# Performance work log

Measured on AMD Instinct MI355X. Metric: run time of the kernel, lower is better.

## Reference

```python
import jax, jax.numpy as jnp
import numpy as np

B, S, IN, H = 16, 512, 512, 256
TAU_TRACE = 20.0
TAU_MEM = 20.0
DECAY_TRACE = float(np.exp(-1.0 / TAU_TRACE))  # exp_convolve decay
DECAY_MEM = float(np.exp(-1.0 / TAU_MEM))      # leaky-integrator dynamics decay
LR = 0.01                                       # plasticity learning rate
W_MAX = 1.0                                     # soft upper bound on fast weights


def setup_inputs() -> dict:
    key = jax.random.key(0)
    k1, k2 = jax.random.split(key)
    x = jax.random.normal(k1, (B, S, IN), dtype=jnp.float32)
    # xavier_uniform with gain=sqrt(2) on W of shape [2H, IN]
    lim = float(np.sqrt(2.0) * np.sqrt(6.0 / (2 * H + IN)))
    W = jax.random.uniform(k2, (2 * H, IN), dtype=jnp.float32, minval=-lim, maxval=lim)
    return {"x": x, "W": W}


def reference(x, W):
    # i = x @ W^T : [B, S, 2H], then split into key/value input currents
    i = jnp.einsum('bsi,hi->bsh', x, W)
    ik, iv = jnp.split(i, 2, axis=2)  # each [B, S, H]
    bsz = x.shape[0]
    h = W.shape[0] // 2

    def step(carry, inp):
        kv, vv, kt, vt, mem = carry
        ik_t, iv_t = inp  # [B, H] each
        # key dynamics (leaky integrator + tanh)
        kv = DECAY_MEM * kv + ik_t
        key = jnp.tanh(kv)
        # memory readout: 0.2 * (key.unsqueeze(1) * mem).sum(2) == 0.2 * mem @ key
        ikv = 0.2 * jnp.einsum('bij,bj->bi', mem, key)
        # value dynamics
        vv = DECAY_MEM * vv + iv_t + ikv
        val = jnp.tanh(vv)
        # exponential traces
        kt = DECAY_TRACE * kt + (1.0 - DECAY_TRACE) * key
        vt = DECAY_TRACE * vt + (1.0 - DECAY_TRACE) * val
        # soft-bounded Hebbian outer-product fast-weight update
        mem = mem + LR * (vt[:, :, None] * kt[:, None, :]) * (W_MAX - mem)
        return (kv, vv, kt, vt, mem), (key, val)

    z = jnp.zeros((bsz, h), x.dtype)
    mem0 = jnp.zeros((bsz, h, h), x.dtype)
    (_, _, _, _, mem), (keys, vals) = jax.lax.scan(
        step, (z, z, z, z, mem0),
        (jnp.swapaxes(ik, 0, 1), jnp.swapaxes(iv, 0, 1)))  # scan over time
    return mem, jnp.swapaxes(keys, 0, 1), jnp.swapaxes(vals, 0, 1)
```

## Files before the change

### kernel.cpp

```cpp
#include <hip/hip_runtime.h>

#define BB 16
#define SS 512
#define KIN 512
#define H 256

typedef float v2f __attribute__((ext_vector_type(2)));

constexpr float DECAY = 0.951229424500714f;
constexpr float OMD   = 0.048770575499286f;
constexpr float LR    = 0.01f;

__device__ __forceinline__ float fast_tanh(float x) {
    float e = __expf(2.f * x);
    return 1.f - __fdividef(2.f, e + 1.f);
}

__device__ __forceinline__ v2f pk_mul(v2f a, v2f b) {
    v2f d; asm("v_pk_mul_f32 %0, %1, %2" : "=v"(d) : "v"(a), "v"(b)); return d;
}
__device__ __forceinline__ v2f pk_fma(v2f a, v2f b, v2f c) {
    v2f d; asm("v_pk_fma_f32 %0, %1, %2, %3" : "=v"(d) : "v"(a), "v"(b), "v"(c)); return d;
}

__device__ __forceinline__ void half_sum32(float x, float& s_lo, float& s_hi) {
    int t;
    t = __builtin_amdgcn_update_dpp(0, __float_as_int(x), 0x111, 0xf, 0xf, false);
    x += __int_as_float(t);
    t = __builtin_amdgcn_update_dpp(0, __float_as_int(x), 0x112, 0xf, 0xf, false);
    x += __int_as_float(t);
    t = __builtin_amdgcn_update_dpp(0, __float_as_int(x), 0x114, 0xf, 0xf, false);
    x += __int_as_float(t);
    t = __builtin_amdgcn_update_dpp(0, __float_as_int(x), 0x118, 0xf, 0xf, false);
    x += __int_as_float(t);
    t = __builtin_amdgcn_update_dpp(0, __float_as_int(x), 0x142, 0xa, 0xf, false);
    x += __int_as_float(t);
    s_lo = __int_as_float(__builtin_amdgcn_readlane(__float_as_int(x), 31));
    s_hi = __int_as_float(__builtin_amdgcn_readlane(__float_as_int(x), 63));
}

__global__ __launch_bounds__(256) void gemm_xwT(const float* __restrict__ X,
                                                const float* __restrict__ W,
                                                float* __restrict__ ik_out,
                                                float* __restrict__ iv_t) {
    __shared__ float As[16][68];
    __shared__ float Bs[16][68];
    const int m0 = blockIdx.y * 64;
    const int n0 = blockIdx.x * 64;
    const int tid = threadIdx.x;
    const int r  = tid >> 2;
    const int cg = tid & 3;
    const int tx = tid & 15;
    const int ty = tid >> 4;
    float acc[4][4] = {};
    for (int k0 = 0; k0 < KIN; k0 += 16) {
        float4 av = *(const float4*)&X[(size_t)(m0 + r) * KIN + k0 + cg * 4];
        float4 bv = *(const float4*)&W[(size_t)(n0 + r) * KIN + k0 + cg * 4];
        __syncthreads();
        As[cg*4+0][r] = av.x; As[cg*4+1][r] = av.y; As[cg*4+2][r] = av.z; As[cg*4+3][r] = av.w;
        Bs[cg*4+0][r] = bv.x; Bs[cg*4+1][r] = bv.y; Bs[cg*4+2][r] = bv.z; Bs[cg*4+3][r] = bv.w;
        __syncthreads();
#pragma unroll
        for (int kk = 0; kk < 16; ++kk) {
            float4 a = *(const float4*)&As[kk][ty * 4];
            float4 b = *(const float4*)&Bs[kk][tx * 4];
            float ar[4] = {a.x, a.y, a.z, a.w};
            float br[4] = {b.x, b.y, b.z, b.w};
#pragma unroll
            for (int i = 0; i < 4; ++i)
#pragma unroll
                for (int j = 0; j < 4; ++j) acc[i][j] += ar[i] * br[j];
        }
    }
    if (n0 < 256) {
#pragma unroll
        for (int i = 0; i < 4; ++i) {
            float4 o = make_float4(acc[i][0], acc[i][1], acc[i][2], acc[i][3]);
            *(float4*)&ik_out[(size_t)(m0 + ty * 4 + i) * 256 + n0 + tx * 4] = o;
        }
    } else {
        const int b  = m0 >> 9;
        const int s0 = (m0 & 511) + ty * 4;
#pragma unroll
        for (int j = 0; j < 4; ++j) {
            float4 o = make_float4(acc[0][j], acc[1][j], acc[2][j], acc[3][j]);
            *(float4*)&iv_t[((size_t)b * H + (n0 - 256 + tx * 4 + j)) * SS + s0] = o;
        }
    }
}

__global__ __launch_bounds__(64) void key_scan(const float* __restrict__ ik,
                                               float* __restrict__ keys) {
    const int idx = blockIdx.x * 64 + threadIdx.x;
    const int b   = idx >> 8;
    const int col = idx & 255;
    const float* c  = ik + (size_t)b * SS * 256 + col;
    float* ko = keys + (size_t)b * SS * H + col;
    float kv = 0.f;
    constexpr int D = 32;
    float ib[D];
#pragma unroll
    for (int j = 0; j < D; ++j) ib[j] = c[(size_t)j * 256];
    for (int t = 0; t < SS; t += D) {
#pragma unroll
        for (int j = 0; j < D; ++j) {
            float v = ib[j];
            int tn = t + D + j; if (tn > SS - 1) tn = SS - 1;
            ib[j] = c[(size_t)tn * 256];
            kv = DECAY * kv + v;
            ko[(size_t)(t + j) * H] = fast_tanh(kv);
        }
    }
}

__global__ __launch_bounds__(256) void value_scan(const float* __restrict__ keys,
                                                  const float* __restrict__ iv_t,
                                                  float* __restrict__ mem_out,
                                                  float* __restrict__ vals) {
    const int tid  = threadIdx.x;
    const int wave = tid >> 6;
    const int lane = tid & 63;
    const int half = lane >> 5;
    const int sub  = lane & 31;
    const int b    = blockIdx.x & 15;
    const int rg   = blockIdx.x >> 4;
    const int row  = rg * 8 + wave * 2 + half;
    const int so   = sub * 8;

    const float* kp  = keys + (size_t)b * SS * H + so;
    const float* ivp = iv_t + ((size_t)b * H + row) * SS;
    float* vrow = vals + (size_t)b * SS * H + row;

    const v2f DEC2 = {DECAY, DECAY};
    const v2f OMD2 = {OMD, OMD};
    const v2f ONE2 = {1.f, 1.f};
    const v2f NM12 = {-1.f, -1.f};

    v2f mem2[4] = {{0.f,0.f},{0.f,0.f},{0.f,0.f},{0.f,0.f}};
    v2f ktr[4]  = {{0.f,0.f},{0.f,0.f},{0.f,0.f},{0.f,0.f}};
    float vv = 0.f, vt = 0.f, stash = 0.f;

    v2f kR[8][4];
#pragma unroll
    for (int j = 0; j < 8; ++j)
#pragma unroll
        for (int q = 0; q < 4; ++q)
            kR[j][q] = *(const v2f*)(kp + (size_t)j * H + q * 2);
    kp += 8 * H;

    float4 ivA0 = *(const float4*)(ivp);
    float4 ivA1 = *(const float4*)(ivp + 4);
    float4 ivB0 = *(const float4*)(ivp + 8);
    float4 ivB1 = *(const float4*)(ivp + 12);
    ivp += 16;

#define VS_STEP(J, RELOAD, KOFF)                                               \
    {                                                                          \
        const int SL = (J) & 7;                                                \
        v2f kc0 = kR[SL][0], kc1 = kR[SL][1], kc2 = kR[SL][2], kc3 = kR[SL][3];\
        if (RELOAD) {                                                          \
            kR[SL][0] = *(const v2f*)(kp + (KOFF) * H + 0);                    \
            kR[SL][1] = *(const v2f*)(kp + (KOFF) * H + 2);                    \
            kR[SL][2] = *(const v2f*)(kp + (KOFF) * H + 4);                    \
            kR[SL][3] = *(const v2f*)(kp + (KOFF) * H + 6);                    \
        }                                                                      \
        v2f p2 = pk_mul(mem2[0], kc0);                                         \
        p2 = pk_fma(mem2[1], kc1, p2);                                         \
        p2 = pk_fma(mem2[2], kc2, p2);                                         \
        p2 = pk_fma(mem2[3], kc3, p2);                                         \
        float slo, shi;                                                        \
        half_sum32(p2.x + p2.y, slo, shi);                                     \
        float ps = half ? shi : slo;                                           \
        float civ = ivs[J];                                                    \
        vv = __builtin_fmaf(DECAY, vv, civ);                                   \
        vv = __builtin_fmaf(0.2f, ps, vv);                                     \
        float valv = fast_tanh(vv);                                            \
        vt = __builtin_fmaf(DECAY, vt, OMD * valv);                            \
        if (sub == (J)) stash = valv;                                          \
        float c = LR * vt;                                                     \
        v2f c2 = {c, c};                                                       \
        ktr[0] = pk_fma(DEC2, ktr[0], pk_mul(OMD2, kc0));                      \
        ktr[1] = pk_fma(DEC2, ktr[1], pk_mul(OMD2, kc1));                      \
        ktr[2] = pk_fma(DEC2, ktr[2], pk_mul(OMD2, kc2));                      \
        ktr[3] = pk_fma(DEC2, ktr[3], pk_mul(OMD2, kc3));                      \
        v2f d0 = pk_fma(mem2[0], NM12, ONE2);                                  \
        v2f d1 = pk_fma(mem2[1], NM12, ONE2);                                  \
        v2f d2 = pk_fma(mem2[2], NM12, ONE2);                                  \
        v2f d3 = pk_fma(mem2[3], NM12, ONE2);                                  \
        mem2[0] = pk_fma(pk_mul(c2, ktr[0]), d0, mem2[0]);                     \
        mem2[1] = pk_fma(pk_mul(c2, ktr[1]), d1, mem2[1]);                     \
        mem2[2] = pk_fma(pk_mul(c2, ktr[2]), d2, mem2[2]);                     \
        mem2[3] = pk_fma(pk_mul(c2, ktr[3]), d3, mem2[3]);                     \
    }

#define VS_TILE16(RELOAD_A, RELOAD_B)                                          \
    {                                                                          \
        float ivs[16] = {ivA0.x, ivA0.y, ivA0.z, ivA0.w,                       \
                         ivA1.x, ivA1.y, ivA1.z, ivA1.w,                       \
                         ivB0.x, ivB0.y, ivB0.z, ivB0.w,                       \
                         ivB1.x, ivB1.y, ivB1.z, ivB1.w};                      \
        VS_STEP(0, RELOAD_A, 0) VS_STEP(1, RELOAD_A, 1)                        \
        VS_STEP(2, RELOAD_A, 2) VS_STEP(3, RELOAD_A, 3)                        \
        if (RELOAD_A) kp += 4 * H;                                             \
        VS_STEP(4, RELOAD_A, 0) VS_STEP(5, RELOAD_A, 1)                        \
        VS_STEP(6, RELOAD_A, 2) VS_STEP(7, RELOAD_A, 3)                        \
        if (RELOAD_A) kp += 4 * H;                                             \
        VS_STEP(8, RELOAD_B, 0) VS_STEP(9, RELOAD_B, 1)                        \
        VS_STEP(10, RELOAD_B, 2) VS_STEP(11, RELOAD_B, 3)                      \
        if (RELOAD_B) kp += 4 * H;                                             \
        VS_STEP(12, RELOAD_B, 0) VS_STEP(13, RELOAD_B, 1)                      \
        VS_STEP(14, RELOAD_B, 2) VS_STEP(15, RELOAD_B, 3)                      \
        if (RELOAD_B) kp += 4 * H;                                             \
        if (sub < 16) vrow[(size_t)sub * H] = stash;                           \
        vrow += 16 * H;                                                        \
    }

    for (int t0 = 0; t0 < SS - 16; t0 += 16) {
        float4 nA0 = *(const float4*)(ivp);
        float4 nA1 = *(const float4*)(ivp + 4);
        float4 nB0 = *(const float4*)(ivp + 8);
        float4 nB1 = *(const float4*)(ivp + 12);
        ivp += 16;
        VS_TILE16(true, true)
        ivA0 = nA0; ivA1 = nA1; ivB0 = nB0; ivB1 = nB1;
    }
    VS_TILE16(true, false)
#undef VS_TILE16
#undef VS_STEP

    float* mo = &mem_out[((size_t)b * H + row) * H + so];
    *(float4*)&mo[0] = make_float4(mem2[0].x, mem2[0].y, mem2[1].x, mem2[1].y);
    *(float4*)&mo[4] = make_float4(mem2[2].x, mem2[2].y, mem2[3].x, mem2[3].y);
}

extern "C" void kernel_launch(void* const* d_in, const int* in_sizes, int n_in,
                              void* d_out, int out_size, void* d_ws, size_t ws_size,
                              hipStream_t stream) {
    const float* x = (const float*)d_in[0];
    const float* W = (const float*)d_in[1];
    float* out = (float*)d_out;
    float* mem_out = out;
    float* keys = out + (size_t)BB * H * H;
    float* vals = keys + (size_t)BB * SS * H;
    float* ik   = (float*)d_ws;
    float* iv_t = ik + (size_t)BB * SS * 256;

    dim3 gb(8, 128);
    gemm_xwT<<<gb, 256, 0, stream>>>(x, W, ik, iv_t);
    key_scan<<<64, 64, 0, stream>>>(ik, keys);
    value_scan<<<512, 256, 0, stream>>>(keys, iv_t, mem_out, vals);
}
```

Before: 255.1 us.

## Stage key tiles through double-buffered LDS in value_scan instead of per-lane global reloads

The value scan now loads each 16-step tile of keys once per block with coalesced float4 global loads. It writes the tile into a double-buffered shared-memory array in a permuted layout, and each lane reads its 8-element key slice from LDS through a two-slot register ring. Before, every lane kept an 8-step register window and reloaded its slice from global memory, so the 8 rows of a block fetched the same keys redundantly. The change also adds a __syncthreads per tile and a minimum-occupancy hint of 2 blocks per SM. These cost barrier stalls and LDS latency on the serial recurrence, and may constrain register allocation.

```diff
diff --git a/kernel.cpp b/kernel.cpp
--- a/kernel.cpp
+++ b/kernel.cpp
@@ -113,10 +113,11 @@
     }
 }
 
-__global__ __launch_bounds__(256) void value_scan(const float* __restrict__ keys,
-                                                  const float* __restrict__ iv_t,
-                                                  float* __restrict__ mem_out,
-                                                  float* __restrict__ vals) {
+__global__ __launch_bounds__(256, 2) void value_scan(const float* __restrict__ keys,
+                                                     const float* __restrict__ iv_t,
+                                                     float* __restrict__ mem_out,
+                                                     float* __restrict__ vals) {
+    __shared__ float klds[2][16][256];
     const int tid  = threadIdx.x;
     const int wave = tid >> 6;
     const int lane = tid & 63;
@@ -125,9 +126,13 @@
     const int b    = blockIdx.x & 15;
     const int rg   = blockIdx.x >> 4;
     const int row  = rg * 8 + wave * 2 + half;
-    const int so   = sub * 8;
-
-    const float* kp  = keys + (size_t)b * SS * H + so;
+    const int sub2 = sub * 2;
+    const int lane4 = lane * 4;
+    const int s2   = (lane >> 1) * 2;
+    const int q2a  = (lane * 2) & 3;
+    const int q2b  = (lane * 2 + 1) & 3;
+
+    const float* kb  = keys + (size_t)b * SS * H;
     const float* ivp = iv_t + ((size_t)b * H + row) * SS;
     float* vrow = vals + (size_t)b * SS * H + row;
 
@@ -139,31 +144,42 @@
     v2f mem2[4] = {{0.f,0.f},{0.f,0.f},{0.f,0.f},{0.f,0.f}};
     v2f ktr[4]  = {{0.f,0.f},{0.f,0.f},{0.f,0.f},{0.f,0.f}};
     float vv = 0.f, vt = 0.f, stash = 0.f;
-
-    v2f kR[8][4];
-#pragma unroll
-    for (int j = 0; j < 8; ++j)
-#pragma unroll
-        for (int q = 0; q < 4; ++q)
-            kR[j][q] = *(const v2f*)(kp + (size_t)j * H + q * 2);
-    kp += 8 * H;
-
-    float4 ivA0 = *(const float4*)(ivp);
-    float4 ivA1 = *(const float4*)(ivp + 4);
-    float4 ivB0 = *(const float4*)(ivp + 8);
-    float4 ivB1 = *(const float4*)(ivp + 12);
-    ivp += 16;
-
-#define VS_STEP(J, RELOAD, KOFF)                                               \
+    v2f ring[2][4];
+    float4 g0, g1, g2, g3;
+
+#define LOADG(TI) {                                                            \
+        const float* gp_ = kb + (size_t)((TI) * 16 + wave * 4) * H + lane4;    \
+        g0 = *(const float4*)(gp_);                                            \
+        g1 = *(const float4*)(gp_ + H);                                        \
+        g2 = *(const float4*)(gp_ + 2 * H);                                    \
+        g3 = *(const float4*)(gp_ + 3 * H);                                    \
+    }
+
+#define STAGE(BUF) {                                                           \
+        float* rb_ = &klds[BUF][wave * 4][0];                                  \
+        *(v2f*)(rb_ + q2a * 64 + s2)       = v2f{g0.x, g0.y};                  \
+        *(v2f*)(rb_ + q2b * 64 + s2)       = v2f{g0.z, g0.w};                  \
+        *(v2f*)(rb_ + 256 + q2a * 64 + s2) = v2f{g1.x, g1.y};                  \
+        *(v2f*)(rb_ + 256 + q2b * 64 + s2) = v2f{g1.z, g1.w};                  \
+        *(v2f*)(rb_ + 512 + q2a * 64 + s2) = v2f{g2.x, g2.y};                  \
+        *(v2f*)(rb_ + 512 + q2b * 64 + s2) = v2f{g2.z, g2.w};                  \
+        *(v2f*)(rb_ + 768 + q2a * 64 + s2) = v2f{g3.x, g3.y};                  \
+        *(v2f*)(rb_ + 768 + q2b * 64 + s2) = v2f{g3.z, g3.w};                  \
+    }
+
+#define RD(J, SLOT) {                                                          \
+        const float* r_ = &klds[cur][J][sub2];                                 \
+        ring[SLOT][0] = *(const v2f*)(r_);                                     \
+        ring[SLOT][1] = *(const v2f*)(r_ + 64);                                \
+        ring[SLOT][2] = *(const v2f*)(r_ + 128);                               \
+        ring[SLOT][3] = *(const v2f*)(r_ + 192);                               \
+    }
+
+#define VS_STEP(J)                                                             \
     {                                                                          \
-        const int SL = (J) & 7;                                                \
-        v2f kc0 = kR[SL][0], kc1 = kR[SL][1], kc2 = kR[SL][2], kc3 = kR[SL][3];\
-        if (RELOAD) {                                                          \
-            kR[SL][0] = *(const v2f*)(kp + (KOFF) * H + 0);                    \
-            kR[SL][1] = *(const v2f*)(kp + (KOFF) * H + 2);                    \
-            kR[SL][2] = *(const v2f*)(kp + (KOFF) * H + 4);                    \
-            kR[SL][3] = *(const v2f*)(kp + (KOFF) * H + 6);                    \
-        }                                                                      \
+        v2f kc0 = ring[(J)&1][0], kc1 = ring[(J)&1][1],                        \
+            kc2 = ring[(J)&1][2], kc3 = ring[(J)&1][3];                        \
+        if ((J) < 14) RD((J) + 2, (J)&1);                                      \
         v2f p2 = pk_mul(mem2[0], kc0);                                         \
         p2 = pk_fma(mem2[1], kc1, p2);                                         \
         p2 = pk_fma(mem2[2], kc2, p2);                                         \
@@ -171,8 +187,7 @@
         float slo, shi;                                                        \
         half_sum32(p2.x + p2.y, slo, shi);                                     \
         float ps = half ? shi : slo;                                           \
-        float civ = ivs[J];                                                    \
-        vv = __builtin_fmaf(DECAY, vv, civ);                                   \
+        vv = __builtin_fmaf(DECAY, vv, ivs[J]);                                \
         vv = __builtin_fmaf(0.2f, ps, vv);                                     \
         float valv = fast_tanh(vv);                                            \
         vt = __builtin_fmaf(DECAY, vt, OMD * valv);                            \
@@ -193,42 +208,50 @@
         mem2[3] = pk_fma(pk_mul(c2, ktr[3]), d3, mem2[3]);                     \
     }
 
-#define VS_TILE16(RELOAD_A, RELOAD_B)                                          \
-    {                                                                          \
-        float ivs[16] = {ivA0.x, ivA0.y, ivA0.z, ivA0.w,                       \
-                         ivA1.x, ivA1.y, ivA1.z, ivA1.w,                       \
-                         ivB0.x, ivB0.y, ivB0.z, ivB0.w,                       \
-                         ivB1.x, ivB1.y, ivB1.z, ivB1.w};                      \
-        VS_STEP(0, RELOAD_A, 0) VS_STEP(1, RELOAD_A, 1)                        \
-        VS_STEP(2, RELOAD_A, 2) VS_STEP(3, RELOAD_A, 3)                        \
-        if (RELOAD_A) kp += 4 * H;                                             \
-        VS_STEP(4, RELOAD_A, 0) VS_STEP(5, RELOAD_A, 1)                        \
-        VS_STEP(6, RELOAD_A, 2) VS_STEP(7, RELOAD_A, 3)                        \
-        if (RELOAD_A) kp += 4 * H;                                             \
-        VS_STEP(8, RELOAD_B, 0) VS_STEP(9, RELOAD_B, 1)                        \
-        VS_STEP(10, RELOAD_B, 2) VS_STEP(11, RELOAD_B, 3)                      \
-        if (RELOAD_B) kp += 4 * H;                                             \
-        VS_STEP(12, RELOAD_B, 0) VS_STEP(13, RELOAD_B, 1)                      \
-        VS_STEP(14, RELOAD_B, 2) VS_STEP(15, RELOAD_B, 3)                      \
-        if (RELOAD_B) kp += 4 * H;                                             \
-        if (sub < 16) vrow[(size_t)sub * H] = stash;                           \
-        vrow += 16 * H;                                                        \
-    }
-
-    for (int t0 = 0; t0 < SS - 16; t0 += 16) {
-        float4 nA0 = *(const float4*)(ivp);
-        float4 nA1 = *(const float4*)(ivp + 4);
-        float4 nB0 = *(const float4*)(ivp + 8);
-        float4 nB1 = *(const float4*)(ivp + 12);
+    LOADG(0);
+    STAGE(0);
+    LOADG(1);
+    float4 ivA0 = *(const float4*)(ivp);
+    float4 ivA1 = *(const float4*)(ivp + 4);
+    float4 ivB0 = *(const float4*)(ivp + 8);
+    float4 ivB1 = *(const float4*)(ivp + 12);
+    ivp += 16;
+    __syncthreads();
+
+    int cur = 0;
+    for (int tile = 0; tile < 32; ++tile) {
+        RD(0, 0); RD(1, 1);
+        STAGE(cur ^ 1);
+        int tnext = tile + 2; if (tnext > 31) tnext = 31;
+        LOADG(tnext);
+        const float* ivq = (tile < 31) ? ivp : (ivp - 16);
+        float4 nA0 = *(const float4*)(ivq);
+        float4 nA1 = *(const float4*)(ivq + 4);
+        float4 nB0 = *(const float4*)(ivq + 8);
+        float4 nB1 = *(const float4*)(ivq + 12);
         ivp += 16;
-        VS_TILE16(true, true)
+        {
+            float ivs[16] = {ivA0.x, ivA0.y, ivA0.z, ivA0.w,
+                             ivA1.x, ivA1.y, ivA1.z, ivA1.w,
+                             ivB0.x, ivB0.y, ivB0.z, ivB0.w,
+                             ivB1.x, ivB1.y, ivB1.z, ivB1.w};
+            VS_STEP(0)  VS_STEP(1)  VS_STEP(2)  VS_STEP(3)
+            VS_STEP(4)  VS_STEP(5)  VS_STEP(6)  VS_STEP(7)
+            VS_STEP(8)  VS_STEP(9)  VS_STEP(10) VS_STEP(11)
+            VS_STEP(12) VS_STEP(13) VS_STEP(14) VS_STEP(15)
+        }
+        if (sub < 16) vrow[(size_t)sub * H] = stash;
+        vrow += 16 * H;
         ivA0 = nA0; ivA1 = nA1; ivB0 = nB0; ivB1 = nB1;
-    }
-    VS_TILE16(true, false)
-#undef VS_TILE16
+        __syncthreads();
+        cur ^= 1;
+    }
 #undef VS_STEP
-
-    float* mo = &mem_out[((size_t)b * H + row) * H + so];
+#undef RD
+#undef STAGE
+#undef LOADG
+
+    float* mo = &mem_out[((size_t)b * H + row) * H + sub * 8];
     *(float4*)&mo[0] = make_float4(mem2[0].x, mem2[0].y, mem2[1].x, mem2[1].y);
     *(float4*)&mo[4] = make_float4(mem2[2].x, mem2[2].y, mem2[3].x, mem2[3].y);
 }
```

New measurement: 265.7 us. 1.04x slower.

## Precompute key traces in key_scan and load them in value_scan

Applied to the files above, without the earlier changes.

The key exponential trace is computed once per (batch, column) in key_scan and written in place over the ik workspace. value_scan then loads it instead of recomputing the trace in every row-owning wave, which removes redundant packed FMAs. The half-wave reduction now ends with a ds_swizzle broadcast instead of two readlanes and a select, and launch bounds request 2 blocks per CU. The cost is doubled global loads of key-side data in value_scan, plus more registers for the tR buffer.

```diff
diff --git a/kernel.cpp b/kernel.cpp
--- a/kernel.cpp
+++ b/kernel.cpp
@@ -23,7 +23,7 @@
     v2f d; asm("v_pk_fma_f32 %0, %1, %2, %3" : "=v"(d) : "v"(a), "v"(b), "v"(c)); return d;
 }
 
-__device__ __forceinline__ void half_sum32(float x, float& s_lo, float& s_hi) {
+__device__ __forceinline__ float allred32(float x) {
     int t;
     t = __builtin_amdgcn_update_dpp(0, __float_as_int(x), 0x111, 0xf, 0xf, false);
     x += __int_as_float(t);
@@ -35,8 +35,7 @@
     x += __int_as_float(t);
     t = __builtin_amdgcn_update_dpp(0, __float_as_int(x), 0x142, 0xa, 0xf, false);
     x += __int_as_float(t);
-    s_lo = __int_as_float(__builtin_amdgcn_readlane(__float_as_int(x), 31));
-    s_hi = __int_as_float(__builtin_amdgcn_readlane(__float_as_int(x), 63));
+    return __int_as_float(__builtin_amdgcn_ds_swizzle(__float_as_int(x), 0x3E0));
 }
 
 __global__ __launch_bounds__(256) void gemm_xwT(const float* __restrict__ X,
@@ -89,14 +88,14 @@
     }
 }
 
-__global__ __launch_bounds__(64) void key_scan(const float* __restrict__ ik,
+__global__ __launch_bounds__(64) void key_scan(float* ik,
                                                float* __restrict__ keys) {
     const int idx = blockIdx.x * 64 + threadIdx.x;
     const int b   = idx >> 8;
     const int col = idx & 255;
-    const float* c  = ik + (size_t)b * SS * 256 + col;
+    float* c  = ik + (size_t)b * SS * 256 + col;
     float* ko = keys + (size_t)b * SS * H + col;
-    float kv = 0.f;
+    float kv = 0.f, kt = 0.f;
     constexpr int D = 32;
     float ib[D];
 #pragma unroll
@@ -108,15 +107,19 @@
             int tn = t + D + j; if (tn > SS - 1) tn = SS - 1;
             ib[j] = c[(size_t)tn * 256];
             kv = DECAY * kv + v;
-            ko[(size_t)(t + j) * H] = fast_tanh(kv);
-        }
-    }
-}
-
-__global__ __launch_bounds__(256) void value_scan(const float* __restrict__ keys,
-                                                  const float* __restrict__ iv_t,
-                                                  float* __restrict__ mem_out,
-                                                  float* __restrict__ vals) {
+            float key = fast_tanh(kv);
+            kt = __builtin_fmaf(DECAY, kt, OMD * key);
+            ko[(size_t)(t + j) * H] = key;
+            c[(size_t)(t + j) * 256] = kt;
+        }
+    }
+}
+
+__global__ __launch_bounds__(256, 2) void value_scan(const float* __restrict__ keys,
+                                                     const float* __restrict__ kts,
+                                                     const float* __restrict__ iv_t,
+                                                     float* __restrict__ mem_out,
+                                                     float* __restrict__ vals) {
     const int tid  = threadIdx.x;
     const int wave = tid >> 6;
     const int lane = tid & 63;
@@ -128,104 +131,108 @@
     const int so   = sub * 8;
 
     const float* kp  = keys + (size_t)b * SS * H + so;
+    const float* tp  = kts  + (size_t)b * SS * H + so;
     const float* ivp = iv_t + ((size_t)b * H + row) * SS;
     float* vrow = vals + (size_t)b * SS * H + row;
 
-    const v2f DEC2 = {DECAY, DECAY};
-    const v2f OMD2 = {OMD, OMD};
     const v2f ONE2 = {1.f, 1.f};
     const v2f NM12 = {-1.f, -1.f};
 
     v2f mem2[4] = {{0.f,0.f},{0.f,0.f},{0.f,0.f},{0.f,0.f}};
-    v2f ktr[4]  = {{0.f,0.f},{0.f,0.f},{0.f,0.f},{0.f,0.f}};
     float vv = 0.f, vt = 0.f, stash = 0.f;
 
-    v2f kR[8][4];
+    v2f kR[8][4], tR[8][4];
 #pragma unroll
     for (int j = 0; j < 8; ++j)
 #pragma unroll
-        for (int q = 0; q < 4; ++q)
+        for (int q = 0; q < 4; ++q) {
             kR[j][q] = *(const v2f*)(kp + (size_t)j * H + q * 2);
-    kp += 8 * H;
-
-    float4 ivA0 = *(const float4*)(ivp);
-    float4 ivA1 = *(const float4*)(ivp + 4);
-    float4 ivB0 = *(const float4*)(ivp + 8);
-    float4 ivB1 = *(const float4*)(ivp + 12);
+            tR[j][q] = *(const v2f*)(tp + (size_t)j * H + q * 2);
+        }
+    const float* kpF = kp + 8 * H;
+    const float* tpF = tp + 8 * H;
+
+    float4 iA0 = *(const float4*)(ivp + 0);
+    float4 iA1 = *(const float4*)(ivp + 4);
+    float4 iB0 = *(const float4*)(ivp + 8);
+    float4 iB1 = *(const float4*)(ivp + 12);
     ivp += 16;
 
-#define VS_STEP(J, RELOAD, KOFF)                                               \
+#define VS_STEP(J, RELOAD)                                                     \
     {                                                                          \
-        const int SL = (J) & 7;                                                \
-        v2f kc0 = kR[SL][0], kc1 = kR[SL][1], kc2 = kR[SL][2], kc3 = kR[SL][3];\
+        v2f kc0 = kR[(J)&7][0], kc1 = kR[(J)&7][1],                            \
+            kc2 = kR[(J)&7][2], kc3 = kR[(J)&7][3];                            \
+        v2f tc0 = tR[(J)&7][0], tc1 = tR[(J)&7][1],                            \
+            tc2 = tR[(J)&7][2], tc3 = tR[(J)&7][3];                            \
         if (RELOAD) {                                                          \
-            kR[SL][0] = *(const v2f*)(kp + (KOFF) * H + 0);                    \
-            kR[SL][1] = *(const v2f*)(kp + (KOFF) * H + 2);                    \
-            kR[SL][2] = *(const v2f*)(kp + (KOFF) * H + 4);                    \
-            kR[SL][3] = *(const v2f*)(kp + (KOFF) * H + 6);                    \
+            kR[(J)&7][0] = *(const v2f*)(kpF + ((J)&3) * H + 0);               \
+            kR[(J)&7][1] = *(const v2f*)(kpF + ((J)&3) * H + 2);               \
+            kR[(J)&7][2] = *(const v2f*)(kpF + ((J)&3) * H + 4);               \
+            kR[(J)&7][3] = *(const v2f*)(kpF + ((J)&3) * H + 6);               \
+            tR[(J)&7][0] = *(const v2f*)(tpF + ((J)&3) * H + 0);               \
+            tR[(J)&7][1] = *(const v2f*)(tpF + ((J)&3) * H + 2);               \
+            tR[(J)&7][2] = *(const v2f*)(tpF + ((J)&3) * H + 4);               \
+            tR[(J)&7][3] = *(const v2f*)(tpF + ((J)&3) * H + 6);               \
         }                                                                      \
         v2f p2 = pk_mul(mem2[0], kc0);                                         \
         p2 = pk_fma(mem2[1], kc1, p2);                                         \
         p2 = pk_fma(mem2[2], kc2, p2);                                         \
         p2 = pk_fma(mem2[3], kc3, p2);                                         \
-        float slo, shi;                                                        \
-        half_sum32(p2.x + p2.y, slo, shi);                                     \
-        float ps = half ? shi : slo;                                           \
-        float civ = ivs[J];                                                    \
-        vv = __builtin_fmaf(DECAY, vv, civ);                                   \
-        vv = __builtin_fmaf(0.2f, ps, vv);                                     \
+        float s = allred32(p2.x + p2.y);                                       \
+        vv = __builtin_fmaf(DECAY, vv, ivs[J]);                                \
+        vv = __builtin_fmaf(0.2f, s, vv);                                      \
         float valv = fast_tanh(vv);                                            \
         vt = __builtin_fmaf(DECAY, vt, OMD * valv);                            \
         if (sub == (J)) stash = valv;                                          \
         float c = LR * vt;                                                     \
         v2f c2 = {c, c};                                                       \
-        ktr[0] = pk_fma(DEC2, ktr[0], pk_mul(OMD2, kc0));                      \
-        ktr[1] = pk_fma(DEC2, ktr[1], pk_mul(OMD2, kc1));                      \
-        ktr[2] = pk_fma(DEC2, ktr[2], pk_mul(OMD2, kc2));                      \
-        ktr[3] = pk_fma(DEC2, ktr[3], pk_mul(OMD2, kc3));                      \
         v2f d0 = pk_fma(mem2[0], NM12, ONE2);                                  \
         v2f d1 = pk_fma(mem2[1], NM12, ONE2);                                  \
         v2f d2 = pk_fma(mem2[2], NM12, ONE2);                                  \
         v2f d3 = pk_fma(mem2[3], NM12, ONE2);                                  \
-        mem2[0] = pk_fma(pk_mul(c2, ktr[0]), d0, mem2[0]);                     \
-        mem2[1] = pk_fma(pk_mul(c2, ktr[1]), d1, mem2[1]);                     \
-        mem2[2] = pk_fma(pk_mul(c2, ktr[2]), d2, mem2[2]);                     \
-        mem2[3] = pk_fma(pk_mul(c2, ktr[3]), d3, mem2[3]);                     \
-    }
-
-#define VS_TILE16(RELOAD_A, RELOAD_B)                                          \
-    {                                                                          \
-        float ivs[16] = {ivA0.x, ivA0.y, ivA0.z, ivA0.w,                       \
-                         ivA1.x, ivA1.y, ivA1.z, ivA1.w,                       \
-                         ivB0.x, ivB0.y, ivB0.z, ivB0.w,                       \
-                         ivB1.x, ivB1.y, ivB1.z, ivB1.w};                      \
-        VS_STEP(0, RELOAD_A, 0) VS_STEP(1, RELOAD_A, 1)                        \
-        VS_STEP(2, RELOAD_A, 2) VS_STEP(3, RELOAD_A, 3)                        \
-        if (RELOAD_A) kp += 4 * H;                                             \
-        VS_STEP(4, RELOAD_A, 0) VS_STEP(5, RELOAD_A, 1)                        \
-        VS_STEP(6, RELOAD_A, 2) VS_STEP(7, RELOAD_A, 3)                        \
-        if (RELOAD_A) kp += 4 * H;                                             \
-        VS_STEP(8, RELOAD_B, 0) VS_STEP(9, RELOAD_B, 1)                        \
-        VS_STEP(10, RELOAD_B, 2) VS_STEP(11, RELOAD_B, 3)                      \
-        if (RELOAD_B) kp += 4 * H;                                             \
-        VS_STEP(12, RELOAD_B, 0) VS_STEP(13, RELOAD_B, 1)                      \
-        VS_STEP(14, RELOAD_B, 2) VS_STEP(15, RELOAD_B, 3)                      \
-        if (RELOAD_B) kp += 4 * H;                                             \
-        if (sub < 16) vrow[(size_t)sub * H] = stash;                           \
-        vrow += 16 * H;                                                        \
+        mem2[0] = pk_fma(pk_mul(c2, tc0), d0, mem2[0]);                        \
+        mem2[1] = pk_fma(pk_mul(c2, tc1), d1, mem2[1]);                        \
+        mem2[2] = pk_fma(pk_mul(c2, tc2), d2, mem2[2]);                        \
+        mem2[3] = pk_fma(pk_mul(c2, tc3), d3, mem2[3]);                        \
+        asm volatile("" ::: "memory");                                         \
     }
 
     for (int t0 = 0; t0 < SS - 16; t0 += 16) {
-        float4 nA0 = *(const float4*)(ivp);
+        float4 nA0 = *(const float4*)(ivp + 0);
         float4 nA1 = *(const float4*)(ivp + 4);
         float4 nB0 = *(const float4*)(ivp + 8);
         float4 nB1 = *(const float4*)(ivp + 12);
         ivp += 16;
-        VS_TILE16(true, true)
-        ivA0 = nA0; ivA1 = nA1; ivB0 = nB0; ivB1 = nB1;
-    }
-    VS_TILE16(true, false)
-#undef VS_TILE16
+        {
+            float ivs[16] = {iA0.x, iA0.y, iA0.z, iA0.w,
+                             iA1.x, iA1.y, iA1.z, iA1.w,
+                             iB0.x, iB0.y, iB0.z, iB0.w,
+                             iB1.x, iB1.y, iB1.z, iB1.w};
+            VS_STEP(0, 1)  VS_STEP(1, 1)  VS_STEP(2, 1)  VS_STEP(3, 1)
+            kpF += 4 * H; tpF += 4 * H;
+            VS_STEP(4, 1)  VS_STEP(5, 1)  VS_STEP(6, 1)  VS_STEP(7, 1)
+            kpF += 4 * H; tpF += 4 * H;
+            VS_STEP(8, 1)  VS_STEP(9, 1)  VS_STEP(10, 1) VS_STEP(11, 1)
+            kpF += 4 * H; tpF += 4 * H;
+            VS_STEP(12, 1) VS_STEP(13, 1) VS_STEP(14, 1) VS_STEP(15, 1)
+            kpF += 4 * H; tpF += 4 * H;
+        }
+        if (sub < 16) vrow[(size_t)sub * H] = stash;
+        vrow += 16 * H;
+        iA0 = nA0; iA1 = nA1; iB0 = nB0; iB1 = nB1;
+    }
+    {
+        float ivs[16] = {iA0.x, iA0.y, iA0.z, iA0.w,
+                         iA1.x, iA1.y, iA1.z, iA1.w,
+                         iB0.x, iB0.y, iB0.z, iB0.w,
+                         iB1.x, iB1.y, iB1.z, iB1.w};
+        VS_STEP(0, 1)  VS_STEP(1, 1)  VS_STEP(2, 1)  VS_STEP(3, 1)
+        kpF += 4 * H; tpF += 4 * H;
+        VS_STEP(4, 1)  VS_STEP(5, 1)  VS_STEP(6, 1)  VS_STEP(7, 1)
+        VS_STEP(8, 0)  VS_STEP(9, 0)  VS_STEP(10, 0) VS_STEP(11, 0)
+        VS_STEP(12, 0) VS_STEP(13, 0) VS_STEP(14, 0) VS_STEP(15, 0)
+        if (sub < 16) vrow[(size_t)sub * H] = stash;
+    }
 #undef VS_STEP
 
     float* mo = &mem_out[((size_t)b * H + row) * H + so];
@@ -248,5 +255,5 @@
     dim3 gb(8, 128);
     gemm_xwT<<<gb, 256, 0, stream>>>(x, W, ik, iv_t);
     key_scan<<<64, 64, 0, stream>>>(ik, keys);
-    value_scan<<<512, 256, 0, stream>>>(keys, iv_t, mem_out, vals);
-}
+    value_scan<<<512, 256, 0, stream>>>(keys, ik, iv_t, mem_out, vals);
+}
```

Result: slower. 266.7 us (+4.6%).
